# Kernel tuning notes

Measured on AMD Instinct MI355X. Metric: run time of the kernel, lower is better.

## Reference

```python
import jax, jax.numpy as jnp
import numpy as np

N_NODES = 100000
N_EDGES = 1000000
D_IN = 256
D_OUT = 64


def setup_inputs() -> dict:
    key = jax.random.key(0)
    k1, k2, k3, k4, k5, k6 = jax.random.split(key, 6)
    x = jax.random.normal(k1, (N_NODES, D_IN), dtype=jnp.float32)
    # Xavier-style uniform init: stdv = 1/sqrt(output_dim)
    stdv = 1.0 / np.sqrt(D_OUT)
    weight = jax.random.uniform(k2, (D_IN, D_OUT), dtype=jnp.float32, minval=-stdv, maxval=stdv)
    adj_vals = jax.random.uniform(k3, (N_EDGES,), dtype=jnp.float32)
    prelu_a = jnp.full((1,), 0.25, dtype=jnp.float32)  # nn.PReLU default
    row = jax.random.randint(k4, (N_EDGES,), 0, N_NODES, dtype=jnp.int32)
    col = jax.random.randint(k5, (N_EDGES,), 0, N_NODES, dtype=jnp.int32)
    return {"x": x, "weight": weight, "adj_vals": adj_vals, "prelu_a": prelu_a,
            "row": row, "col": col}


def reference(x, weight, adj_vals, prelu_a, row, col):
    # dense GEMM: [N, D_in] @ [D_in, D_out]
    hidden = x @ weight  # gc_drop=0 -> identity dropout
    # sparse adj spmm: out[i] = sum_{e: row[e]=i} adj_vals[e] * hidden[col[e]]
    msg = adj_vals[:, None] * hidden[col]  # [E, D_out]
    agg = jax.ops.segment_sum(msg, row, num_segments=N_NODES)  # [N, D_out]
    # PReLU with single shared slope
    out = jnp.where(agg > 0, agg, prelu_a * agg)
    return out
```

## Files before the change

kernel.cpp:

```cpp
#include <hip/hip_runtime.h>

#define N_NODES 100000
#define N_EDGES 1000000
#define D_IN    256
#define D_OUT   64

#define BKT_SHIFT   8
#define NODES_PER_B 256
#define N_BKT       391
#define BKT_CAP     3072
#define EPB         8192
#define BIN_BLOCKS  123
#define GEMM_BLOCKS 782
#define NUM_TILES   6250

#define CUR_STRIDE  32

typedef __attribute__((ext_vector_type(8))) short short8;
typedef __attribute__((ext_vector_type(4))) float f32x4;

__device__ __forceinline__ unsigned short f2bf(float f) {
    unsigned int u = __float_as_uint(f);
    u = (u + 0x7fffu + ((u >> 16) & 1u)) >> 16;
    return (unsigned short)u;
}

__device__ __forceinline__ void mfma_store_tile(
    const short8 afrag[8], const unsigned short wT[64][272],
    unsigned short* __restrict__ hiddenBf, int r0, int n16, int quad)
{
    f32x4 acc[4] = {{0.f,0.f,0.f,0.f},{0.f,0.f,0.f,0.f},
                    {0.f,0.f,0.f,0.f},{0.f,0.f,0.f,0.f}};
#pragma unroll
    for (int ct = 0; ct < 4; ++ct) {
#pragma unroll
        for (int kk = 0; kk < 8; ++kk) {
            short8 b = *(const short8*)&wT[ct * 16 + n16][kk * 32 + quad * 8];
            acc[ct] = __builtin_amdgcn_mfma_f32_16x16x32_bf16(
                afrag[kk], b, acc[ct], 0, 0, 0);
        }
    }
#pragma unroll
    for (int ct = 0; ct < 4; ++ct)
#pragma unroll
        for (int reg = 0; reg < 4; ++reg)
            hiddenBf[(size_t)(r0 + quad * 4 + reg) * D_OUT + ct * 16 + n16]
                = f2bf(acc[ct][reg]);
}

__global__ __launch_bounds__(256, 2) void gemm_bin_kernel(
    const float* __restrict__ x, const float* __restrict__ w,
    unsigned short* __restrict__ hiddenBf,
    const int* __restrict__ row, const int* __restrict__ col,
    const float* __restrict__ adj, int* __restrict__ gCursor,
    int2* __restrict__ edges)
{
    const int t = threadIdx.x;

    if (blockIdx.x < BIN_BLOCKS) {
        __shared__ int cnt[N_BKT];
        __shared__ int cbase[N_BKT];
        __shared__ int cur[N_BKT];

        const int e0 = blockIdx.x * EPB;

        for (int i = t; i < N_BKT; i += 256) cnt[i] = 0;
        __syncthreads();

        int rreg[32];
#pragma unroll
        for (int u = 0; u < 32; ++u) {
            int e = e0 + t + u * 256;
            rreg[u] = (e < N_EDGES) ? row[e] : -1;
        }
#pragma unroll
        for (int u = 0; u < 32; ++u)
            if (rreg[u] >= 0) atomicAdd(&cnt[rreg[u] >> BKT_SHIFT], 1);
        __syncthreads();

        for (int i = t; i < N_BKT; i += 256) {
            int c = cnt[i];
            cbase[i] = c ? atomicAdd(&gCursor[i * CUR_STRIDE], c) : 0;
            cur[i] = 0;
        }
        __syncthreads();

#pragma unroll
        for (int u0 = 0; u0 < 32; u0 += 8) {
            int   cc[8]; float vv[8];
#pragma unroll
            for (int u = 0; u < 8; ++u) {
                int e = e0 + t + (u0 + u) * 256;
                if (rreg[u0 + u] >= 0) { cc[u] = col[e]; vv[u] = adj[e]; }
                else                   { cc[u] = 0;      vv[u] = 0.f;    }
            }
#pragma unroll
            for (int u = 0; u < 8; ++u) {
                int r = rreg[u0 + u];
                if (r >= 0) {
                    int b = r >> BKT_SHIFT;
                    int off = cbase[b] + atomicAdd(&cur[b], 1);
                    if (off < BKT_CAP) {
                        edges[b * BKT_CAP + off] =
                            make_int2(((r & (NODES_PER_B - 1)) << 17) | cc[u],
                                      __float_as_int(vv[u]));
                    }
                }
            }
        }
        return;
    }

    __shared__ unsigned short wT[64][272];

    for (int i = 0; i < 64; ++i) {
        int idx = t + i * 256;
        int k = idx >> 6, n = idx & 63;
        wT[n][k] = f2bf(w[idx]);
    }
    __syncthreads();

    const int lane = t & 63;
    const int wid  = t >> 6;
    const int n16  = lane & 15;
    const int quad = lane >> 4;

    const int waveGid = (blockIdx.x - BIN_BLOCKS) * 4 + wid;
    const int t0 = waveGid * 2;
    if (t0 >= NUM_TILES) return;

    float4 lo[8], hi[8];
    short8 afrag[8];

    {
        const float* xrow = x + (size_t)(t0 * 16 + n16) * D_IN + quad * 8;
#pragma unroll
        for (int kk = 0; kk < 8; ++kk) {
            lo[kk] = *(const float4*)(xrow + kk * 32);
            hi[kk] = *(const float4*)(xrow + kk * 32 + 4);
        }
    }
#pragma unroll
    for (int kk = 0; kk < 8; ++kk) {
        short8 a;
        a[0] = (short)f2bf(lo[kk].x); a[1] = (short)f2bf(lo[kk].y);
        a[2] = (short)f2bf(lo[kk].z); a[3] = (short)f2bf(lo[kk].w);
        a[4] = (short)f2bf(hi[kk].x); a[5] = (short)f2bf(hi[kk].y);
        a[6] = (short)f2bf(hi[kk].z); a[7] = (short)f2bf(hi[kk].w);
        afrag[kk] = a;
    }

    const int t1 = t0 + 1;
    const bool have1 = t1 < NUM_TILES;
    if (have1) {
        const float* xrow = x + (size_t)(t1 * 16 + n16) * D_IN + quad * 8;
#pragma unroll
        for (int kk = 0; kk < 8; ++kk) {
            lo[kk] = *(const float4*)(xrow + kk * 32);
            hi[kk] = *(const float4*)(xrow + kk * 32 + 4);
        }
    }

    mfma_store_tile(afrag, wT, hiddenBf, t0 * 16, n16, quad);

    if (have1) {
#pragma unroll
        for (int kk = 0; kk < 8; ++kk) {
            short8 a;
            a[0] = (short)f2bf(lo[kk].x); a[1] = (short)f2bf(lo[kk].y);
            a[2] = (short)f2bf(lo[kk].z); a[3] = (short)f2bf(lo[kk].w);
            a[4] = (short)f2bf(hi[kk].x); a[5] = (short)f2bf(hi[kk].y);
            a[6] = (short)f2bf(hi[kk].z); a[7] = (short)f2bf(hi[kk].w);
            afrag[kk] = a;
        }
        mfma_store_tile(afrag, wT, hiddenBf, t1 * 16, n16, quad);
    }
}

__global__ __launch_bounds__(512) void csr_kernel(
    const int2* __restrict__ edges, const int* __restrict__ gCursor,
    int2* __restrict__ csr, unsigned int* __restrict__ startdeg)
{
    __shared__ int cnt[NODES_PER_B];
    __shared__ int cur[NODES_PER_B];

    const int b = blockIdx.x, t = threadIdx.x;
    if (t < NODES_PER_B) cnt[t] = 0;
    __syncthreads();

    const int base = b * BKT_CAP;
    int size = gCursor[b * CUR_STRIDE];
    if (size > BKT_CAP) size = BKT_CAP;

    for (int i = t; i < size; i += 512)
        atomicAdd(&cnt[(unsigned)edges[base + i].x >> 17], 1);
    __syncthreads();

    int v = (t < NODES_PER_B) ? cnt[t] : 0;
    for (int off = 1; off < NODES_PER_B; off <<= 1) {
        int tmp = (t < NODES_PER_B && t >= off) ? cnt[t - off] : 0;
        __syncthreads();
        if (t < NODES_PER_B) cnt[t] += tmp;
        __syncthreads();
    }
    if (t < NODES_PER_B) {
        int gstart = base + cnt[t] - v;
        cur[t] = gstart;
        int node = b * NODES_PER_B + t;
        if (node < N_NODES)
            startdeg[node] = ((unsigned)gstart << 11) |
                             (unsigned)(v < 2047 ? v : 2047);
    }
    __syncthreads();

    for (int i = t; i < size; i += 512) {
        int2 rec = edges[base + i];
        int rl = (unsigned)rec.x >> 17;
        int pos = atomicAdd(&cur[rl], 1);
        csr[pos] = make_int2(rec.x & 0x1FFFF, rec.y);
    }
}

__global__ __launch_bounds__(256) void agg_kernel(
    const unsigned short* __restrict__ hiddenBf,
    const unsigned int* __restrict__ startdeg,
    const int2* __restrict__ csr, const float* __restrict__ prelu_a,
    float* __restrict__ out)
{
    const int wid  = threadIdx.x >> 6;
    const int lane = threadIdx.x & 63;
    const int node = blockIdx.x * 4 + wid;

    const unsigned int sd = startdeg[node];
    const int start = sd >> 11;
    const int deg   = sd & 2047;

    float acc = 0.f;
    for (int base = 0; base < deg; base += 64) {
        int take = deg - base;
        if (take > 64) take = 64;
        int2 rec = make_int2(0, 0);
        if (lane < take) rec = csr[start + base + lane];

        int j = 0;
        for (; j + 8 <= take; j += 8) {
            int   c[8]; float v[8]; float h[8];
#pragma unroll
            for (int u = 0; u < 8; ++u) {
                c[u] = __builtin_amdgcn_readlane(rec.x, j + u);
                v[u] = __int_as_float(__builtin_amdgcn_readlane(rec.y, j + u));
            }
#pragma unroll
            for (int u = 0; u < 8; ++u)
                h[u] = __uint_as_float(
                    (unsigned)hiddenBf[(size_t)c[u] * D_OUT + lane] << 16);
#pragma unroll
            for (int u = 0; u < 8; ++u) acc += v[u] * h[u];
        }
        for (; j < take; ++j) {
            int   c = __builtin_amdgcn_readlane(rec.x, j);
            float v = __int_as_float(__builtin_amdgcn_readlane(rec.y, j));
            float h = __uint_as_float(
                (unsigned)hiddenBf[(size_t)c * D_OUT + lane] << 16);
            acc += v * h;
        }
    }
    const float a = prelu_a[0];
    out[(size_t)node * D_OUT + lane] = acc > 0.f ? acc : a * acc;
}

extern "C" void kernel_launch(void* const* d_in, const int* in_sizes, int n_in,
                              void* d_out, int out_size, void* d_ws, size_t ws_size,
                              hipStream_t stream)
{
    const float* x       = (const float*)d_in[0];
    const float* w       = (const float*)d_in[1];
    const float* adj     = (const float*)d_in[2];
    const float* prelu_a = (const float*)d_in[3];
    const int*   row     = (const int*)d_in[4];
    const int*   col     = (const int*)d_in[5];
    float* out = (float*)d_out;

    char* ws = (char*)d_ws;
    unsigned short* hiddenBf = (unsigned short*)(ws);
    int2*  edges    = (int2*)        (ws + 12800000);
    int2*  csr      = (int2*)        (ws + 22409216);
    unsigned int* startdeg = (unsigned int*)(ws + 32018944);
    int*   gCursor  = (int*)         (ws + 32419328);

    hipMemsetAsync(gCursor, 0, N_BKT * CUR_STRIDE * sizeof(int), stream);

    gemm_bin_kernel<<<BIN_BLOCKS + GEMM_BLOCKS, 256, 0, stream>>>(
        x, w, hiddenBf, row, col, adj, gCursor, edges);

    csr_kernel<<<N_BKT, 512, 0, stream>>>(edges, gCursor, csr, startdeg);

    agg_kernel<<<N_NODES / 4, 256, 0, stream>>>(hiddenBf, startdeg, csr, prelu_a, out);
}
```

Baseline: 244.5 us.

## Fuse CSR build and aggregation into per-bucket LDS atomic accumulation

Removes the CSR construction kernel and the per-node aggregation kernel. A single kernel now walks each 256-node bucket's edges directly and accumulates weighted hidden rows into a 64KB shared-memory accumulator with LDS atomics, then applies PReLU and writes the output. This avoids the CSR write/read round trip and one launch. In exchange it adds float atomics on shared memory and makes accumulation order nondeterministic. The grid drops to only 391 blocks with large LDS use, so occupancy may be low.

```diff
diff --git a/kernel.cpp b/kernel.cpp
--- a/kernel.cpp
+++ b/kernel.cpp
@@ -177,96 +177,73 @@
     }
 }
 
-__global__ __launch_bounds__(512) void csr_kernel(
+__global__ __launch_bounds__(512, 2) void bucket_agg_kernel(
+    const unsigned short* __restrict__ hiddenBf,
     const int2* __restrict__ edges, const int* __restrict__ gCursor,
-    int2* __restrict__ csr, unsigned int* __restrict__ startdeg)
-{
-    __shared__ int cnt[NODES_PER_B];
-    __shared__ int cur[NODES_PER_B];
-
-    const int b = blockIdx.x, t = threadIdx.x;
-    if (t < NODES_PER_B) cnt[t] = 0;
+    const float* __restrict__ prelu_a, float* __restrict__ out)
+{
+    __shared__ float acc[NODES_PER_B * D_OUT];
+
+    const int b    = blockIdx.x;
+    const int t    = threadIdx.x;
+    const int lane = t & 63;
+    const int wid  = t >> 6;
+
+    float4* az = (float4*)acc;
+#pragma unroll
+    for (int i = 0; i < 8; ++i)
+        az[t + i * 512] = make_float4(0.f, 0.f, 0.f, 0.f);
     __syncthreads();
 
     const int base = b * BKT_CAP;
     int size = gCursor[b * CUR_STRIDE];
     if (size > BKT_CAP) size = BKT_CAP;
 
-    for (int i = t; i < size; i += 512)
-        atomicAdd(&cnt[(unsigned)edges[base + i].x >> 17], 1);
-    __syncthreads();
-
-    int v = (t < NODES_PER_B) ? cnt[t] : 0;
-    for (int off = 1; off < NODES_PER_B; off <<= 1) {
-        int tmp = (t < NODES_PER_B && t >= off) ? cnt[t - off] : 0;
-        __syncthreads();
-        if (t < NODES_PER_B) cnt[t] += tmp;
-        __syncthreads();
-    }
-    if (t < NODES_PER_B) {
-        int gstart = base + cnt[t] - v;
-        cur[t] = gstart;
-        int node = b * NODES_PER_B + t;
-        if (node < N_NODES)
-            startdeg[node] = ((unsigned)gstart << 11) |
-                             (unsigned)(v < 2047 ? v : 2047);
-    }
-    __syncthreads();
-
-    for (int i = t; i < size; i += 512) {
-        int2 rec = edges[base + i];
-        int rl = (unsigned)rec.x >> 17;
-        int pos = atomicAdd(&cur[rl], 1);
-        csr[pos] = make_int2(rec.x & 0x1FFFF, rec.y);
-    }
-}
-
-__global__ __launch_bounds__(256) void agg_kernel(
-    const unsigned short* __restrict__ hiddenBf,
-    const unsigned int* __restrict__ startdeg,
-    const int2* __restrict__ csr, const float* __restrict__ prelu_a,
-    float* __restrict__ out)
-{
-    const int wid  = threadIdx.x >> 6;
-    const int lane = threadIdx.x & 63;
-    const int node = blockIdx.x * 4 + wid;
-
-    const unsigned int sd = startdeg[node];
-    const int start = sd >> 11;
-    const int deg   = sd & 2047;
-
-    float acc = 0.f;
-    for (int base = 0; base < deg; base += 64) {
-        int take = deg - base;
+    for (int i0 = wid * 64; i0 < size; i0 += 512) {
+        int take = size - i0;
         if (take > 64) take = 64;
         int2 rec = make_int2(0, 0);
-        if (lane < take) rec = csr[start + base + lane];
+        if (lane < take) rec = edges[base + i0 + lane];
 
         int j = 0;
         for (; j + 8 <= take; j += 8) {
-            int   c[8]; float v[8]; float h[8];
+            int nl[8]; int c[8]; float v[8]; float h[8];
 #pragma unroll
             for (int u = 0; u < 8; ++u) {
-                c[u] = __builtin_amdgcn_readlane(rec.x, j + u);
-                v[u] = __int_as_float(__builtin_amdgcn_readlane(rec.y, j + u));
+                int rx = __builtin_amdgcn_readlane(rec.x, j + u);
+                nl[u] = rx >> 17;
+                c[u]  = rx & 0x1FFFF;
+                v[u]  = __int_as_float(__builtin_amdgcn_readlane(rec.y, j + u));
             }
 #pragma unroll
             for (int u = 0; u < 8; ++u)
                 h[u] = __uint_as_float(
                     (unsigned)hiddenBf[(size_t)c[u] * D_OUT + lane] << 16);
 #pragma unroll
-            for (int u = 0; u < 8; ++u) acc += v[u] * h[u];
+            for (int u = 0; u < 8; ++u)
+                atomicAdd(&acc[nl[u] * D_OUT + lane], v[u] * h[u]);
         }
         for (; j < take; ++j) {
-            int   c = __builtin_amdgcn_readlane(rec.x, j);
+            int rx = __builtin_amdgcn_readlane(rec.x, j);
             float v = __int_as_float(__builtin_amdgcn_readlane(rec.y, j));
             float h = __uint_as_float(
-                (unsigned)hiddenBf[(size_t)c * D_OUT + lane] << 16);
-            acc += v * h;
-        }
-    }
+                (unsigned)hiddenBf[(size_t)(rx & 0x1FFFF) * D_OUT + lane] << 16);
+            atomicAdd(&acc[(rx >> 17) * D_OUT + lane], v * h);
+        }
+    }
+    __syncthreads();
+
     const float a = prelu_a[0];
-    out[(size_t)node * D_OUT + lane] = acc > 0.f ? acc : a * acc;
+    const int node0 = b * NODES_PER_B;
+#pragma unroll
+    for (int i = 0; i < 32; ++i) {
+        int idx  = t + i * 512;
+        int node = node0 + (idx >> 6);
+        if (node < N_NODES) {
+            float s = acc[idx];
+            out[(size_t)node * D_OUT + (idx & 63)] = s > 0.f ? s : a * s;
+        }
+    }
 }
 
 extern "C" void kernel_launch(void* const* d_in, const int* in_sizes, int n_in,
@@ -284,16 +261,13 @@
     char* ws = (char*)d_ws;
     unsigned short* hiddenBf = (unsigned short*)(ws);
     int2*  edges    = (int2*)        (ws + 12800000);
-    int2*  csr      = (int2*)        (ws + 22409216);
-    unsigned int* startdeg = (unsigned int*)(ws + 32018944);
-    int*   gCursor  = (int*)         (ws + 32419328);
+    int*   gCursor  = (int*)         (ws + 22409216);
 
     hipMemsetAsync(gCursor, 0, N_BKT * CUR_STRIDE * sizeof(int), stream);
 
     gemm_bin_kernel<<<BIN_BLOCKS + GEMM_BLOCKS, 256, 0, stream>>>(
         x, w, hiddenBf, row, col, adj, gCursor, edges);
 
-    csr_kernel<<<N_BKT, 512, 0, stream>>>(edges, gCursor, csr, startdeg);
-
-    agg_kernel<<<N_NODES / 4, 256, 0, stream>>>(hiddenBf, startdeg, csr, prelu_a, out);
-}
+    bucket_agg_kernel<<<N_BKT, 512, 0, stream>>>(
+        hiddenBf, edges, gCursor, prelu_a, out);
+}
```

After: 630.1 us. 158% more time.
